# Kernel tuning notes

Hardware: AMD Instinct MI355X
Metric: run time of the kernel (lower is better)

Reference implementation:

```python
import jax, jax.numpy as jnp
import numpy as np

N_NODES = 50000
N_GRAPHS = 16
NEG_SLOPE = 0.2


def gat_layer(x, W, a_s, a_d, b, src, dst, num_nodes):
    # h: [N, out]
    h = x @ W
    # per-node attention logits (heads=1)
    al_s = (h * a_s).sum(-1)  # [N]
    al_d = (h * a_d).sum(-1)  # [N]
    e = jax.nn.leaky_relu(al_s[src] + al_d[dst], NEG_SLOPE)  # [E]
    # segment softmax over incoming edges of each destination node
    m = jax.ops.segment_max(e, dst, num_segments=num_nodes)
    p = jnp.exp(e - m[dst])
    z = jax.ops.segment_sum(p, dst, num_segments=num_nodes)
    coef = p / z[dst]  # self-loops guarantee z > 0
    out = jax.ops.segment_sum(coef[:, None] * h[src], dst, num_segments=num_nodes)
    return out + b


def setup_inputs() -> dict:
    key = jax.random.key(0)
    ks = jax.random.split(key, 20)
    in_dim, hid, out_dim = 256, 128, 128
    E = 800000
    x = jax.random.normal(ks[0], (N_NODES, in_dim), dtype=jnp.float32)
    edge_index = jax.random.randint(ks[1], (2, E), 0, N_NODES, dtype=jnp.int32)
    batch = jnp.sort(jax.random.randint(ks[2], (N_NODES,), 0, N_GRAPHS, dtype=jnp.int32))

    def glorot(k, shape):
        fan = shape[0] + shape[-1]
        s = jnp.sqrt(6.0 / fan)
        return jax.random.uniform(k, shape, jnp.float32, -s, s)

    dims = [(in_dim, hid), (hid, hid), (hid, out_dim)]
    inp = {"x": x, "edge_index": edge_index, "batch": batch}
    for i, (di, do) in enumerate(dims):
        inp[f"W{i}"] = glorot(ks[3 + 4 * i], (di, do))
        inp[f"as{i}"] = glorot(ks[4 + 4 * i], (1, do))[0]
        inp[f"ad{i}"] = glorot(ks[5 + 4 * i], (1, do))[0]
        inp[f"b{i}"] = jnp.zeros((do,), jnp.float32)
    return inp


def reference(x, edge_index, batch, W0, as0, ad0, b0, W1, as1, ad1, b1, W2, as2, ad2, b2):
    # add self loops once (PyG GATConv add_self_loops=True)
    loops = jnp.arange(N_NODES, dtype=edge_index.dtype)
    src = jnp.concatenate([edge_index[0], loops])
    dst = jnp.concatenate([edge_index[1], loops])

    h = gat_layer(x, W0, as0, ad0, b0, src, dst, N_NODES)
    h = jax.nn.relu(h)  # act; dropout is identity at eval
    h = gat_layer(h, W1, as1, ad1, b1, src, dst, N_NODES)
    h = jax.nn.relu(h)
    node_emb = gat_layer(h, W2, as2, ad2, b2, src, dst, N_NODES)

    # global_mean_pool
    b32 = batch.astype(jnp.int32)
    sums = jax.ops.segment_sum(node_emb, b32, num_segments=N_GRAPHS)
    cnt = jax.ops.segment_sum(jnp.ones((N_NODES,), node_emb.dtype), b32, num_segments=N_GRAPHS)
    return sums / jnp.maximum(cnt, 1.0)[:, None]
```

## Files before the change

kernel.cpp:

```cpp
#include <hip/hip_runtime.h>
#include <math.h>

#define NN 50000
#define NE 800000
#define NTE (NE + NN)
#define NG 16
#define HID 128
#define NEG_SLOPE 0.2f

#define NBUK 391
#define SLOT 2560
#define EPW 4096
#define NWG_E ((NTE + EPW - 1) / EPW)
#define GEMM_GRID ((NN + 63) / 64)

#define BPAD 136
#define SMEM_BYTES 34816

typedef __attribute__((ext_vector_type(8))) __bf16 bf16x8;
typedef __attribute__((ext_vector_type(4))) float f32x4;

union V16 {
    float4 f4;
    uint4 u4;
    bf16x8 b8;
    __bf16 h[8];
};

__global__ void k_prep(int* __restrict__ bwr, float* __restrict__ sums,
                       int* __restrict__ off,
                       const float* __restrict__ W0, const float* __restrict__ W1,
                       const float* __restrict__ W2, __bf16* __restrict__ Wt0,
                       __bf16* __restrict__ Wt1, __bf16* __restrict__ Wt2) {
    int t = blockIdx.x * blockDim.x + threadIdx.x;
    if (t == 0) off[NN] = NTE;
    if (t <= NBUK) bwr[t] = 0;
    if (t < NG * HID) sums[t] = 0.0f;
    if (t < 256 * HID) {
        int k = t >> 7, n = t & 127;
        Wt0[(size_t)n * 256 + k] = (__bf16)W0[t];
    } else if (t < 256 * HID + HID * HID) {
        int u = t - 256 * HID;
        int k = u >> 7, n = u & 127;
        Wt1[(size_t)n * HID + k] = (__bf16)W1[u];
    } else if (t < 256 * HID + 2 * HID * HID) {
        int u = t - 256 * HID - HID * HID;
        int k = u >> 7, n = u & 127;
        Wt2[(size_t)n * HID + k] = (__bf16)W2[u];
    }
}

__device__ __forceinline__ void scatter_body(const int* __restrict__ ei,
                                             int* __restrict__ bwr,
                                             int* __restrict__ rec, int blk,
                                             char* smem) {
    int* hist = (int*)smem;
    int* cur = hist + NBUK;
    int t = threadIdx.x;
    for (int b = t; b < NBUK; b += 256) hist[b] = 0;
    __syncthreads();
    int base = blk * EPW;
    #pragma unroll
    for (int r = 0; r < EPW / 256; r++) {
        int idx = base + r * 256 + t;
        if (idx < NTE) {
            int dst = (idx < NE) ? ei[NE + idx] : (idx - NE);
            atomicAdd(&hist[dst >> 7], 1);
        }
    }
    __syncthreads();
    for (int b = t; b < NBUK; b += 256) {
        int c = hist[b];
        if (c) cur[b] = atomicAdd(&bwr[b], c);
    }
    __syncthreads();
    #pragma unroll
    for (int r = 0; r < EPW / 256; r++) {
        int idx = base + r * 256 + t;
        if (idx < NTE) {
            int src, dst;
            if (idx < NE) { src = ei[idx]; dst = ei[NE + idx]; }
            else          { src = idx - NE; dst = src; }
            int b = dst >> 7;
            int pos = atomicAdd(&cur[b], 1);
            rec[(size_t)b * SLOT + pos] = src | ((dst & 127) << 17);
        }
    }
}

__device__ __forceinline__ void scan512(const int* __restrict__ bwr, int* s) {
    int t = threadIdx.x;
    s[t] = (t < NBUK) ? bwr[t] : 0;
    s[t + 256] = (t + 256 < NBUK) ? bwr[t + 256] : 0;
    __syncthreads();
    for (int o = 1; o < 512; o <<= 1) {
        int a0 = (t >= o) ? s[t - o] : 0;
        int a1 = s[t + 256 - o];
        __syncthreads();
        s[t] += a0;
        s[t + 256] += a1;
        __syncthreads();
    }
}

__global__ __launch_bounds__(256) void k_bfill(const int* __restrict__ bwr,
                                               const int* __restrict__ rec,
                                               int* __restrict__ off,
                                               int* __restrict__ csr) {
    __shared__ int s[512];
    __shared__ int cnt[128];
    __shared__ int scn[128];
    __shared__ int cur[128];
    int b = blockIdx.x, t = threadIdx.x;
    scan512(bwr, s);
    int base = s[b] - bwr[b];
    int n = bwr[b];
    const int* rb = rec + (size_t)b * SLOT;
    if (t < 128) cnt[t] = 0;
    __syncthreads();
    for (int i = t; i < n; i += 256) atomicAdd(&cnt[rb[i] >> 17], 1);
    __syncthreads();
    if (t < 128) scn[t] = cnt[t];
    __syncthreads();
    #pragma unroll
    for (int o = 1; o < 128; o <<= 1) {
        int add = (t >= o && t < 128) ? scn[t - o] : 0;
        __syncthreads();
        if (t < 128) scn[t] += add;
        __syncthreads();
    }
    if (t < 128) {
        int ex = scn[t] - cnt[t];
        cur[t] = ex;
        int d = b * 128 + t;
        if (d < NN) off[d] = base + ex;
    }
    __syncthreads();
    for (int i = t; i < n; i += 256) {
        int r = rb[i];
        int dloc = r >> 17;
        int src = r & 131071;
        int pos = atomicAdd(&cur[dloc], 1);
        csr[base + pos] = src;
    }
}

template <typename AT, int K>
__device__ __forceinline__ void gemm_body(const AT* __restrict__ A,
                                          const __bf16* __restrict__ Bt,
                                          __bf16* __restrict__ C,
                                          const float* __restrict__ a_s,
                                          const float* __restrict__ a_d,
                                          float* __restrict__ als,
                                          float* __restrict__ ald,
                                          int M, int blk, char* smem) {
    __bf16(*Bs)[BPAD] = (__bf16(*)[BPAD])smem;

    int tid = threadIdx.x;
    int rowBase = blk * 64;
    int wv = tid >> 6;
    int lane = tid & 63;
    int g = lane >> 4;
    int c = lane & 15;

    int rowA = rowBase + wv * 16 + c;
    bool va = rowA < M;

    f32x4 acc[8];
    #pragma unroll
    for (int ni = 0; ni < 8; ni++) acc[ni] = (f32x4){0.f, 0.f, 0.f, 0.f};

    for (int kh = 0; kh < K; kh += 128) {
        if (kh) __syncthreads();
        #pragma unroll
        for (int rep = 0; rep < 8; rep++) {
            int ch = rep * 256 + tid;
            int r = ch >> 4, q = ch & 15;
            *(float4*)&Bs[r][q * 8] = *(const float4*)(Bt + (size_t)r * K + kh + q * 8);
        }
        bf16x8 afr[4];
        #pragma unroll
        for (int kc = 0; kc < 4; kc++) {
            if constexpr (sizeof(AT) == 2) {
                V16 t;
                t.f4 = (float4){0.f, 0.f, 0.f, 0.f};
                if (va) t.f4 = *(const float4*)((const __bf16*)A + (size_t)rowA * K + kh + kc * 32 + g * 8);
                afr[kc] = t.b8;
            } else {
                float vv[8] = {0.f, 0.f, 0.f, 0.f, 0.f, 0.f, 0.f, 0.f};
                if (va) {
                    const float* Ap = (const float*)A + (size_t)rowA * K + kh + kc * 32 + g * 8;
                    float4 v0 = *(const float4*)Ap;
                    float4 v1 = *(const float4*)(Ap + 4);
                    vv[0] = v0.x; vv[1] = v0.y; vv[2] = v0.z; vv[3] = v0.w;
                    vv[4] = v1.x; vv[5] = v1.y; vv[6] = v1.z; vv[7] = v1.w;
                }
                V16 t;
                #pragma unroll
                for (int q = 0; q < 8; q++) t.h[q] = (__bf16)vv[q];
                afr[kc] = t.b8;
            }
        }
        __syncthreads();

        #pragma unroll
        for (int kc = 0; kc < 4; kc++) {
            #pragma unroll
            for (int ni = 0; ni < 8; ni++) {
                bf16x8 b = *(const bf16x8*)&Bs[ni * 16 + c][kc * 32 + g * 8];
                acc[ni] = __builtin_amdgcn_mfma_f32_16x16x32_bf16(afr[kc], b, acc[ni], 0, 0, 0);
            }
        }
    }

    float asv[8], adv[8];
    #pragma unroll
    for (int ni = 0; ni < 8; ni++) {
        asv[ni] = a_s[ni * 16 + c];
        adv[ni] = a_d[ni * 16 + c];
    }
    int rb = rowBase + wv * 16 + g * 4;
    #pragma unroll
    for (int i = 0; i < 4; i++) {
        int row = rb + i;
        float s = 0.f, dd = 0.f;
        #pragma unroll
        for (int ni = 0; ni < 8; ni++) {
            float v = acc[ni][i];
            s = fmaf(v, asv[ni], s);
            dd = fmaf(v, adv[ni], dd);
        }
        #pragma unroll
        for (int o = 1; o <= 8; o <<= 1) {
            s += __shfl_xor(s, o);
            dd += __shfl_xor(dd, o);
        }
        if (row < M) {
            #pragma unroll
            for (int ni = 0; ni < 8; ni++)
                C[(size_t)row * HID + ni * 16 + c] = (__bf16)acc[ni][i];
            if (c == 0) {
                als[row] = s;
                ald[row] = dd;
            }
        }
    }
}

__global__ __launch_bounds__(256, 4) void k_gemm_bf16(const __bf16* __restrict__ A,
                                                      const __bf16* __restrict__ Bt,
                                                      __bf16* __restrict__ C,
                                                      const float* __restrict__ a_s,
                                                      const float* __restrict__ a_d,
                                                      float* __restrict__ als,
                                                      float* __restrict__ ald) {
    __shared__ __align__(16) char smem[SMEM_BYTES];
    gemm_body<__bf16, HID>(A, Bt, C, a_s, a_d, als, ald, NN, blockIdx.x, smem);
}

__global__ __launch_bounds__(256, 4) void k_gemm0_scatter(const float* __restrict__ x,
                                                          const __bf16* __restrict__ Wt0,
                                                          __bf16* __restrict__ C,
                                                          const float* __restrict__ a_s,
                                                          const float* __restrict__ a_d,
                                                          float* __restrict__ als,
                                                          float* __restrict__ ald,
                                                          const int* __restrict__ ei,
                                                          int* __restrict__ bwr,
                                                          int* __restrict__ rec) {
    __shared__ __align__(16) char smem[SMEM_BYTES];
    if (blockIdx.x < GEMM_GRID) {
        gemm_body<float, 256>(x, Wt0, C, a_s, a_d, als, ald, NN, blockIdx.x, smem);
    } else {
        scatter_body(ei, bwr, rec, blockIdx.x - GEMM_GRID, smem);
    }
}

__global__ __launch_bounds__(256) void k_attn(const __bf16* __restrict__ h,
                                              const float* __restrict__ als,
                                              const float* __restrict__ ald,
                                              const int* __restrict__ off,
                                              const int* __restrict__ csr,
                                              const float* __restrict__ bias,
                                              __bf16* __restrict__ yout,
                                              const int* __restrict__ batch,
                                              float* __restrict__ sums,
                                              int do_relu, int do_pool) {
    __shared__ float py[8][128];
    __shared__ int pg[8];
    int tid = threadIdx.x;
    int w = (blockIdx.x * blockDim.x + tid) >> 6;
    int lane = tid & 63;
    int half = lane >> 5;
    int l32 = lane & 31;
    int gn = (lane >> 4) & 1;
    int c = lane & 15;
    int d = 2 * w + half;

    int e0 = off[d], e1 = off[d + 1];
    int deg = e1 - e0;
    float ald_d = ald[d];
    float acc[8] = {0.f, 0.f, 0.f, 0.f, 0.f, 0.f, 0.f, 0.f};

    if (deg <= 32) {
        int s = 0;
        float e = -INFINITY;
        if (l32 < deg) {
            s = csr[e0 + l32];
            float t = als[s] + ald_d;
            e = (t > 0.0f) ? t : NEG_SLOPE * t;
        }
        float mx = e;
        #pragma unroll
        for (int o = 16; o > 0; o >>= 1) mx = fmaxf(mx, __shfl_xor(mx, o));
        float p = (l32 < deg) ? __expf(e - mx) : 0.0f;
        float z = p;
        #pragma unroll
        for (int o = 16; o > 0; o >>= 1) z += __shfl_xor(z, o);
        float cf = p * (1.0f / z);

        int degR = (deg + 1) & ~1;
        #pragma unroll 4
        for (int k = gn; k < degR; k += 2) {
            int srcl = (half << 5) + k;
            int ss = __shfl(s, srcl);
            float cw = __shfl(cf, srcl);
            V16 v;
            v.f4 = *(const float4*)(h + (size_t)ss * HID + c * 8);
            #pragma unroll
            for (int i = 0; i < 4; i++) {
                unsigned int u = (&v.u4.x)[i];
                float lo = __uint_as_float(u << 16);
                float hi = __uint_as_float(u & 0xffff0000u);
                acc[2 * i]     = fmaf(cw, lo, acc[2 * i]);
                acc[2 * i + 1] = fmaf(cw, hi, acc[2 * i + 1]);
            }
        }
    } else {
        float mx = -INFINITY;
        for (int j = e0 + l32; j < e1; j += 32) {
            float t = als[csr[j]] + ald_d;
            t = (t > 0.0f) ? t : NEG_SLOPE * t;
            mx = fmaxf(mx, t);
        }
        #pragma unroll
        for (int o = 16; o > 0; o >>= 1) mx = fmaxf(mx, __shfl_xor(mx, o));
        float z = 0.0f;
        for (int j = e0 + l32; j < e1; j += 32) {
            float t = als[csr[j]] + ald_d;
            t = (t > 0.0f) ? t : NEG_SLOPE * t;
            z += __expf(t - mx);
        }
        #pragma unroll
        for (int o = 16; o > 0; o >>= 1) z += __shfl_xor(z, o);
        float inv_z = 1.0f / z;
        for (int k = gn; k < deg; k += 2) {
            int ss = csr[e0 + k];
            float t = als[ss] + ald_d;
            t = (t > 0.0f) ? t : NEG_SLOPE * t;
            float cw = __expf(t - mx) * inv_z;
            V16 v;
            v.f4 = *(const float4*)(h + (size_t)ss * HID + c * 8);
            #pragma unroll
            for (int i = 0; i < 4; i++) {
                unsigned int u = (&v.u4.x)[i];
                float lo = __uint_as_float(u << 16);
                float hi = __uint_as_float(u & 0xffff0000u);
                acc[2 * i]     = fmaf(cw, lo, acc[2 * i]);
                acc[2 * i + 1] = fmaf(cw, hi, acc[2 * i + 1]);
            }
        }
    }

    #pragma unroll
    for (int t = 0; t < 8; t++) acc[t] += __shfl_xor(acc[t], 16);

    if (l32 < 16) {
        float4 b0 = *(const float4*)(bias + c * 8);
        float4 b1 = *(const float4*)(bias + c * 8 + 4);
        acc[0] += b0.x; acc[1] += b0.y; acc[2] += b0.z; acc[3] += b0.w;
        acc[4] += b1.x; acc[5] += b1.y; acc[6] += b1.z; acc[7] += b1.w;
        if (do_relu) {
            #pragma unroll
            for (int t = 0; t < 8; t++) acc[t] = fmaxf(acc[t], 0.0f);
        }
        if (!do_pool) {
            V16 o;
            #pragma unroll
            for (int t = 0; t < 8; t++) o.h[t] = (__bf16)acc[t];
            *(float4*)(yout + (size_t)d * HID + c * 8) = o.f4;
        } else {
            int nib = (tid >> 6) * 2 + half;
            #pragma unroll
            for (int t = 0; t < 8; t++) py[nib][c * 8 + t] = acc[t];
            if (c == 0) pg[nib] = batch[d];
        }
    }
    if (do_pool) {
        __syncthreads();
        if (tid < 128) {
            float a = 0.0f;
            int gc = pg[0];
            #pragma unroll
            for (int n = 0; n < 8; n++) {
                int g = pg[n];
                if (g != gc) {
                    atomicAdd(&sums[gc * HID + tid], a);
                    a = 0.0f;
                    gc = g;
                }
                a += py[n][tid];
            }
            atomicAdd(&sums[gc * HID + tid], a);
        }
    }
}

__global__ void k_div(const float* __restrict__ sums, const int* __restrict__ batch,
                      float* __restrict__ out) {
    int i = blockIdx.x * blockDim.x + threadIdx.x;
    if (i >= NG * HID) return;
    int g = i >> 7;
    int lo = 0, hi = NN;
    while (lo < hi) { int mid = (lo + hi) >> 1; if (batch[mid] < g) lo = mid + 1; else hi = mid; }
    int lo2 = lo, hi2 = NN;
    while (lo2 < hi2) { int mid = (lo2 + hi2) >> 1; if (batch[mid] < g + 1) lo2 = mid + 1; else hi2 = mid; }
    int c = lo2 - lo;
    out[i] = sums[i] / (float)(c > 1 ? c : 1);
}

extern "C" void kernel_launch(void* const* d_in, const int* in_sizes, int n_in,
                              void* d_out, int out_size, void* d_ws, size_t ws_size,
                              hipStream_t stream) {
    const float* x     = (const float*)d_in[0];
    const int*   ei    = (const int*)d_in[1];
    const int*   batch = (const int*)d_in[2];
    const float* W[3]  = {(const float*)d_in[3], (const float*)d_in[7], (const float*)d_in[11]};
    const float* AS[3] = {(const float*)d_in[4], (const float*)d_in[8], (const float*)d_in[12]};
    const float* AD[3] = {(const float*)d_in[5], (const float*)d_in[9], (const float*)d_in[13]};
    const float* BI[3] = {(const float*)d_in[6], (const float*)d_in[10], (const float*)d_in[14]};
    float* out = (float*)d_out;

    char* ws = (char*)d_ws;
    size_t o = 0;
    auto alloc = [&](size_t bytes) {
        void* p = ws + o;
        o = (o + bytes + 255) & ~(size_t)255;
        return p;
    };
    __bf16* hb  = (__bf16*)alloc((size_t)NN * HID * 2);
    __bf16* yb  = (__bf16*)alloc((size_t)NN * HID * 2);
    __bf16* Wt0 = (__bf16*)alloc((size_t)256 * HID * 2);
    __bf16* Wt1 = (__bf16*)alloc((size_t)HID * HID * 2);
    __bf16* Wt2 = (__bf16*)alloc((size_t)HID * HID * 2);
    float* als  = (float*)alloc(NN * 4);
    float* ald  = (float*)alloc(NN * 4);
    int* off    = (int*)alloc((NN + 1) * 4);
    int* bwr    = (int*)alloc((NBUK + 1) * 4);
    int* rec    = (int*)alloc((size_t)NBUK * SLOT * 4);
    int* csr    = (int*)alloc((size_t)NTE * 4);
    float* sums = (float*)alloc(NG * HID * 4);
    (void)ws_size; (void)in_sizes; (void)n_in; (void)out_size;

    const int attn_grid = (NN / 2) * 64 / 256;

    k_prep<<<(256 * HID + 2 * HID * HID + 255) / 256, 256, 0, stream>>>(
        bwr, sums, off, W[0], W[1], W[2], Wt0, Wt1, Wt2);

    k_gemm0_scatter<<<GEMM_GRID + NWG_E, 256, 0, stream>>>(
        x, Wt0, hb, AS[0], AD[0], als, ald, ei, bwr, rec);

    k_bfill<<<NBUK, 256, 0, stream>>>(bwr, rec, off, csr);

    k_attn<<<attn_grid, 256, 0, stream>>>(hb, als, ald, off, csr, BI[0], yb,
                                          batch, sums, 1, 0);

    k_gemm_bf16<<<GEMM_GRID, 256, 0, stream>>>(yb, Wt1, hb, AS[1], AD[1], als, ald);
    k_attn<<<attn_grid, 256, 0, stream>>>(hb, als, ald, off, csr, BI[1], yb,
                                          batch, sums, 1, 0);

    k_gemm_bf16<<<GEMM_GRID, 256, 0, stream>>>(yb, Wt2, hb, AS[2], AD[2], als, ald);
    k_attn<<<attn_grid, 256, 0, stream>>>(hb, als, ald, off, csr, BI[2], yb,
                                          batch, sums, 0, 1);

    k_div<<<(NG * HID + 255) / 256, 256, 0, stream>>>(sums, batch, out);
}
```

Before: 309.7 us.

## Map one destination node per wavefront with four-way edge-parallel gather

The attention kernel now gives each destination node a full 64-lane wavefront instead of half a wavefront. The lanes split into four 16-lane groups, and each group processes two neighbours per iteration, with edge indices and softmax coefficients staged in LDS rather than broadcast by shuffles. This is meant to raise memory-level parallelism and cut serial per-node latency, since degrees average around 17. The costs are twice as many wavefronts, extra padded gathers of row 0 when degree is rounded up to 8, and one more cross-lane reduction step.

```diff
diff --git a/kernel.cpp b/kernel.cpp
--- a/kernel.cpp
+++ b/kernel.cpp
@@ -286,75 +286,80 @@
                                               const int* __restrict__ batch,
                                               float* __restrict__ sums,
                                               int do_relu, int do_pool) {
-    __shared__ float py[8][128];
-    __shared__ int pg[8];
+    __shared__ int2 s_e[4][64];
+    __shared__ float py[4][128];
+    __shared__ int pg[4];
     int tid = threadIdx.x;
-    int w = (blockIdx.x * blockDim.x + tid) >> 6;
-    int lane = tid & 63;
-    int half = lane >> 5;
-    int l32 = lane & 31;
-    int gn = (lane >> 4) & 1;
+    int gt = blockIdx.x * blockDim.x + tid;
+    int d = gt >> 6;
+    int lane = gt & 63;
+    if (d >= NN) return;
+    int wv = tid >> 6;
+    int grp = lane >> 4;
     int c = lane & 15;
-    int d = 2 * w + half;
 
     int e0 = off[d], e1 = off[d + 1];
     int deg = e1 - e0;
     float ald_d = ald[d];
     float acc[8] = {0.f, 0.f, 0.f, 0.f, 0.f, 0.f, 0.f, 0.f};
 
-    if (deg <= 32) {
+    if (deg <= 64) {
         int s = 0;
         float e = -INFINITY;
-        if (l32 < deg) {
-            s = csr[e0 + l32];
+        if (lane < deg) {
+            s = csr[e0 + lane];
             float t = als[s] + ald_d;
             e = (t > 0.0f) ? t : NEG_SLOPE * t;
         }
         float mx = e;
         #pragma unroll
-        for (int o = 16; o > 0; o >>= 1) mx = fmaxf(mx, __shfl_xor(mx, o));
-        float p = (l32 < deg) ? __expf(e - mx) : 0.0f;
+        for (int o = 32; o > 0; o >>= 1) mx = fmaxf(mx, __shfl_xor(mx, o));
+        float p = (lane < deg) ? __expf(e - mx) : 0.0f;
         float z = p;
         #pragma unroll
-        for (int o = 16; o > 0; o >>= 1) z += __shfl_xor(z, o);
-        float cf = p * (1.0f / z);
-
-        int degR = (deg + 1) & ~1;
-        #pragma unroll 4
-        for (int k = gn; k < degR; k += 2) {
-            int srcl = (half << 5) + k;
-            int ss = __shfl(s, srcl);
-            float cw = __shfl(cf, srcl);
-            V16 v;
-            v.f4 = *(const float4*)(h + (size_t)ss * HID + c * 8);
+        for (int o = 32; o > 0; o >>= 1) z += __shfl_xor(z, o);
+        float inv_z = 1.0f / z;
+        s_e[wv][lane] = make_int2(s, __float_as_int(p * inv_z));
+
+        int degR = (deg + 7) & ~7;
+        #pragma unroll 2
+        for (int k = grp; k < degR; k += 8) {
+            int2 p0 = s_e[wv][k];
+            int2 p1 = s_e[wv][k + 4];
+            float cf0 = __int_as_float(p0.y);
+            float cf1 = __int_as_float(p1.y);
+            V16 v0, v1;
+            v0.f4 = *(const float4*)(h + (size_t)p0.x * HID + c * 8);
+            v1.f4 = *(const float4*)(h + (size_t)p1.x * HID + c * 8);
             #pragma unroll
             for (int i = 0; i < 4; i++) {
-                unsigned int u = (&v.u4.x)[i];
-                float lo = __uint_as_float(u << 16);
-                float hi = __uint_as_float(u & 0xffff0000u);
-                acc[2 * i]     = fmaf(cw, lo, acc[2 * i]);
-                acc[2 * i + 1] = fmaf(cw, hi, acc[2 * i + 1]);
+                unsigned int u0 = (&v0.u4.x)[i];
+                unsigned int u1 = (&v1.u4.x)[i];
+                acc[2 * i]     = fmaf(cf0, __uint_as_float(u0 << 16), acc[2 * i]);
+                acc[2 * i + 1] = fmaf(cf0, __uint_as_float(u0 & 0xffff0000u), acc[2 * i + 1]);
+                acc[2 * i]     = fmaf(cf1, __uint_as_float(u1 << 16), acc[2 * i]);
+                acc[2 * i + 1] = fmaf(cf1, __uint_as_float(u1 & 0xffff0000u), acc[2 * i + 1]);
             }
         }
     } else {
         float mx = -INFINITY;
-        for (int j = e0 + l32; j < e1; j += 32) {
+        for (int j = e0 + lane; j < e1; j += 64) {
             float t = als[csr[j]] + ald_d;
             t = (t > 0.0f) ? t : NEG_SLOPE * t;
             mx = fmaxf(mx, t);
         }
         #pragma unroll
-        for (int o = 16; o > 0; o >>= 1) mx = fmaxf(mx, __shfl_xor(mx, o));
+        for (int o = 32; o > 0; o >>= 1) mx = fmaxf(mx, __shfl_xor(mx, o));
         float z = 0.0f;
-        for (int j = e0 + l32; j < e1; j += 32) {
+        for (int j = e0 + lane; j < e1; j += 64) {
             float t = als[csr[j]] + ald_d;
             t = (t > 0.0f) ? t : NEG_SLOPE * t;
             z += __expf(t - mx);
         }
         #pragma unroll
-        for (int o = 16; o > 0; o >>= 1) z += __shfl_xor(z, o);
+        for (int o = 32; o > 0; o >>= 1) z += __shfl_xor(z, o);
         float inv_z = 1.0f / z;
-        for (int k = gn; k < deg; k += 2) {
+        for (int k = grp; k < deg; k += 4) {
             int ss = csr[e0 + k];
             float t = als[ss] + ald_d;
             t = (t > 0.0f) ? t : NEG_SLOPE * t;
@@ -364,18 +369,19 @@
             #pragma unroll
             for (int i = 0; i < 4; i++) {
                 unsigned int u = (&v.u4.x)[i];
-                float lo = __uint_as_float(u << 16);
-                float hi = __uint_as_float(u & 0xffff0000u);
-                acc[2 * i]     = fmaf(cw, lo, acc[2 * i]);
-                acc[2 * i + 1] = fmaf(cw, hi, acc[2 * i + 1]);
-            }
-        }
-    }
-
-    #pragma unroll
-    for (int t = 0; t < 8; t++) acc[t] += __shfl_xor(acc[t], 16);
-
-    if (l32 < 16) {
+                acc[2 * i]     = fmaf(cw, __uint_as_float(u << 16), acc[2 * i]);
+                acc[2 * i + 1] = fmaf(cw, __uint_as_float(u & 0xffff0000u), acc[2 * i + 1]);
+            }
+        }
+    }
+
+    #pragma unroll
+    for (int t = 0; t < 8; t++) {
+        acc[t] += __shfl_xor(acc[t], 16);
+        acc[t] += __shfl_xor(acc[t], 32);
+    }
+
+    if (grp == 0) {
         float4 b0 = *(const float4*)(bias + c * 8);
         float4 b1 = *(const float4*)(bias + c * 8 + 4);
         acc[0] += b0.x; acc[1] += b0.y; acc[2] += b0.z; acc[3] += b0.w;
@@ -390,10 +396,9 @@
             for (int t = 0; t < 8; t++) o.h[t] = (__bf16)acc[t];
             *(float4*)(yout + (size_t)d * HID + c * 8) = o.f4;
         } else {
-            int nib = (tid >> 6) * 2 + half;
-            #pragma unroll
-            for (int t = 0; t < 8; t++) py[nib][c * 8 + t] = acc[t];
-            if (c == 0) pg[nib] = batch[d];
+            #pragma unroll
+            for (int t = 0; t < 8; t++) py[wv][c * 8 + t] = acc[t];
+            if (c == 0) pg[wv] = batch[d];
         }
     }
     if (do_pool) {
@@ -402,7 +407,7 @@
             float a = 0.0f;
             int gc = pg[0];
             #pragma unroll
-            for (int n = 0; n < 8; n++) {
+            for (int n = 0; n < 4; n++) {
                 int g = pg[n];
                 if (g != gc) {
                     atomicAdd(&sums[gc * HID + tid], a);
@@ -462,7 +467,7 @@
     float* sums = (float*)alloc(NG * HID * 4);
     (void)ws_size; (void)in_sizes; (void)n_in; (void)out_size;
 
-    const int attn_grid = (NN / 2) * 64 / 256;
+    const int attn_grid = (NN * 64 + 255) / 256;
 
     k_prep<<<(256 * HID + 2 * HID * HID + 255) / 256, 256, 0, stream>>>(
         bwr, sums, off, W[0], W[1], W[2], Wt0, Wt1, Wt2);
```

New measurement: 333.4 us. 1.08x slower.
